# Kernel tuning notes

Hardware: AMD Instinct MI355X
Metric: run time of the kernel (lower is better)

Reference implementation:

```python
import jax, jax.numpy as jnp
import numpy as np

N_VARS = 28
HID = 64
BATCH = 32768
BN_EPS = 1e-5


def _lin_init(key, fan_in, shape):
    bound = 1.0 / np.sqrt(fan_in)
    return jax.random.uniform(key, shape, minval=-bound, maxval=bound, dtype=jnp.float32)


def setup_inputs() -> dict:
    key = jax.random.key(0)
    ks = jax.random.split(key, 8)
    n, h = N_VARS, HID
    X = jax.random.normal(ks[0], (BATCH, n), dtype=jnp.float32)
    W_logits = jax.random.uniform(ks[1], (n, n), minval=-0.01, maxval=0.01, dtype=jnp.float32)
    # per-mechanism (grouped) weights, stacked on leading mechanism axis n
    W1 = _lin_init(ks[2], n, (n, h, n)); b1 = _lin_init(ks[3], n, (n, h))
    W2 = _lin_init(ks[4], h, (n, h, h)); b2 = _lin_init(ks[5], h, (n, h))
    W3 = _lin_init(ks[6], h, (n, 1, h)); b3 = _lin_init(ks[7], h, (n, 1))
    gamma1 = jnp.ones((n, h)); beta1 = jnp.zeros((n, h))
    gamma2 = jnp.ones((n, h)); beta2 = jnp.zeros((n, h))
    return {"X": X, "W_logits": W_logits,
            "W1": W1, "b1": b1, "gamma1": gamma1, "beta1": beta1,
            "W2": W2, "b2": b2, "gamma2": gamma2, "beta2": beta2,
            "W3": W3, "b3": b3}


def _bn(x, gamma, beta):
    # x: [n, B, h]; batch stats over B (training-mode BatchNorm1d, biased var)
    m = x.mean(axis=1, keepdims=True)
    v = ((x - m) ** 2).mean(axis=1, keepdims=True)
    return gamma[:, None, :] * (x - m) * jax.lax.rsqrt(v + BN_EPS) + beta[:, None, :]


def reference(X, W_logits, W1, b1, gamma1, beta1, W2, b2, gamma2, beta2, W3, b3):
    n = W_logits.shape[0]
    # adjacency: sigmoid with zeroed diagonal
    W = jax.nn.sigmoid(W_logits) * (1.0 - jnp.eye(n, dtype=W_logits.dtype))
    # fuse the parent mask into the first layer's weights: one grouped GEMM
    # instead of n_vars separate masked matmuls
    W1_eff = W1 * W[:, None, :]                               # [n, h, n]
    h1 = jnp.einsum('bd,nhd->nbh', X, W1_eff) + b1[:, None, :]  # [n, B, h]
    a1 = jax.nn.gelu(_bn(h1, gamma1, beta1), approximate=False)
    h2 = jnp.einsum('nbh,ngh->nbg', a1, W2) + b2[:, None, :]
    a2 = jax.nn.gelu(_bn(h2, gamma2, beta2), approximate=False)
    out = jnp.einsum('nbh,noh->nbo', a2, W3) + b3[:, None, :]   # [n, B, 1]
    X_hat = out[:, :, 0].T                                     # [B, n]
    return (X_hat, W)
```

## Files before the change

### kernel.cpp

```cpp
#include <hip/hip_runtime.h>
#include <hip/hip_bf16.h>
#include <math.h>

typedef float  f4 __attribute__((ext_vector_type(4)));
typedef short  s8 __attribute__((ext_vector_type(8)));
typedef short  s4 __attribute__((ext_vector_type(4)));
typedef int    i2 __attribute__((ext_vector_type(2)));

#define NV 28
#define NB 32768
#define BN_EPS 1e-5f
#define NSLOT 434

#define SUM2_OFF   0
#define SSQ2_OFF   1792
#define BIAS1_OFF  3584
#define PART_OFF   9472
#define BF_BASE_F  120640
#define W2B_OFF_S  57344
#define XBF_OFF_S  172032
#define H2_BYTE_OFF 2924544ull
#define H2_BYTES    117440512ull

__device__ __forceinline__ float gelu_f(float x) {
    float x2 = x * x;
    float z  = x * __builtin_fmaf(x2, -0.10294324f, -2.3022082f);
    float t  = __builtin_amdgcn_exp2f(z);
    return x * __builtin_amdgcn_rcpf(1.0f + t);
}
__device__ __forceinline__ unsigned short f2bf(float x) {
    unsigned u = __builtin_bit_cast(unsigned, x);
    return (unsigned short)((u + 0x7fffu + ((u >> 16) & 1u)) >> 16);
}
__device__ __forceinline__ float bf2f(short s) {
    return __builtin_bit_cast(float, ((int)(unsigned short)s) << 16);
}
__device__ __forceinline__ int bfpack(float a, float b) {
    unsigned ua = __builtin_bit_cast(unsigned, a) + 0x8000u;
    unsigned ub = __builtin_bit_cast(unsigned, b) + 0x8000u;
    return __builtin_amdgcn_perm(ub, ua, 0x07060302);
}
__device__ __forceinline__ float row16_sum(float v) {
    int x;
    x = __builtin_amdgcn_update_dpp(0, __builtin_bit_cast(int, v), 0xB1, 0xF, 0xF, true);
    v += __builtin_bit_cast(float, x);
    x = __builtin_amdgcn_update_dpp(0, __builtin_bit_cast(int, v), 0x4E, 0xF, 0xF, true);
    v += __builtin_bit_cast(float, x);
    x = __builtin_amdgcn_update_dpp(0, __builtin_bit_cast(int, v), 0x124, 0xF, 0xF, true);
    v += __builtin_bit_cast(float, x);
    x = __builtin_amdgcn_update_dpp(0, __builtin_bit_cast(int, v), 0x128, 0xF, 0xF, true);
    v += __builtin_bit_cast(float, x);
    return v;
}
__device__ __forceinline__ float quad4_sum(float v) {
    int x;
    x = __builtin_amdgcn_update_dpp(0, __builtin_bit_cast(int, v), 0xB1, 0xF, 0xF, true);
    v += __builtin_bit_cast(float, x);
    x = __builtin_amdgcn_update_dpp(0, __builtin_bit_cast(int, v), 0x4E, 0xF, 0xF, true);
    v += __builtin_bit_cast(float, x);
    return v;
}

__global__ __launch_bounds__(256) void k_xstats(const float* __restrict__ X,
                                                float* __restrict__ ws) {
    __shared__ float sx[128 * 28];
    const int tid = threadIdx.x;
    const int rowbase = blockIdx.x * 128;
    {
        const f4* src = (const f4*)(X + (size_t)rowbase * 28);
        f4* dst = (f4*)sx;
        for (int i = tid; i < 128 * 28 / 4; i += 256) dst[i] = src[i];
    }
    __syncthreads();
    int* xb = (int*)((short*)(ws + BF_BASE_F) + XBF_OFF_S);
    for (int j = tid; j < 128 * 16; j += 256) {
        int row = j >> 4, cc = j & 15;
        float lo = (2 * cc     < 28) ? sx[row * 28 + 2 * cc]     : 0.0f;
        float hi = (2 * cc + 1 < 28) ? sx[row * 28 + 2 * cc + 1] : 0.0f;
        xb[(size_t)(rowbase + row) * 16 + cc] = (int)f2bf(lo) | ((int)f2bf(hi) << 16);
    }
    for (int s = tid; s < NSLOT; s += 256) {
        float a = 0.0f;
        if (s < 28) {
            for (int r = 0; r < 128; ++r) a += sx[r * 28 + s];
        } else {
            int p = s - 28, d = 0, rem = 28;
            while (p >= rem) { p -= rem; ++d; --rem; }
            int e = d + p;
            for (int r = 0; r < 128; ++r)
                a = __builtin_fmaf(sx[r * 28 + d], sx[r * 28 + e], a);
        }
        ws[PART_OFF + blockIdx.x * NSLOT + s] = a;
    }
}

__global__ __launch_bounds__(256) void k_fold1(const float* __restrict__ Wlog,
                                               const float* __restrict__ W1,
                                               const float* __restrict__ g1,
                                               const float* __restrict__ be1,
                                               const float* __restrict__ W2,
                                               float* __restrict__ ws,
                                               float* __restrict__ out_w) {
    __shared__ float sstat[NSLOT];
    __shared__ float mu[28], wrow[28];
    __shared__ float C[784];
    __shared__ float w1e_s[64 * 28];
    const int n = blockIdx.x, t = threadIdx.x;

    for (int s = t; s < NSLOT; s += 256) {
        float a = 0.0f;
#pragma unroll 16
        for (int p = 0; p < 256; ++p) a += ws[PART_OFF + p * NSLOT + s];
        sstat[s] = a;
    }
    if (t < 64) {
        ws[SUM2_OFF + n * 64 + t] = 0.0f;
        ws[SSQ2_OFF + n * 64 + t] = 0.0f;
    }
    __syncthreads();

    if (t < 28) {
        mu[t] = sstat[t] * (1.0f / 32768.0f);
        float w = 1.0f / (1.0f + expf(-Wlog[n * 28 + t]));
        if (t == n) w = 0.0f;
        wrow[t] = w;
        out_w[n * 28 + t] = w;
    }
    __syncthreads();
    for (int i = t; i < 784; i += 256) {
        int d = i / 28, e = i % 28;
        int lo = d < e ? d : e, hi = d < e ? e : d;
        int idx = 28 + lo * 28 - (lo * (lo - 1)) / 2 + (hi - lo);
        C[i] = sstat[idx] * (1.0f / 32768.0f) - mu[d] * mu[e];
    }
    for (int i = t; i < 1792; i += 256)
        w1e_s[i] = W1[(size_t)n * 1792 + i] * wrow[i % 28];
    __syncthreads();

    const int h = t >> 2, j = t & 3;
    const float* we = &w1e_s[h * 28];
    float var_p = 0.0f, dot_p = 0.0f;
#pragma unroll
    for (int k = 0; k < 7; ++k) {
        int d = 7 * j + k;
        float inner = 0.0f;
#pragma unroll
        for (int e = 0; e < 28; ++e) inner = __builtin_fmaf(C[d * 28 + e], we[e], inner);
        float wd = we[d];
        var_p = __builtin_fmaf(inner, wd, var_p);
        dot_p = __builtin_fmaf(wd, mu[d], dot_p);
    }
    float var  = quad4_sum(var_p);
    float dotm = quad4_sum(dot_p);
    float scale = g1[n * 64 + h] * rsqrtf(fmaxf(var, 0.0f) + BN_EPS);
    if (j == 0)
        ws[BIAS1_OFF + n * 64 + h] = be1[n * 64 + h] - dotm * scale;

    short* bfbase = (short*)(ws + BF_BASE_F);
    {
        short* w1f = bfbase + (size_t)(n * 64 + h) * 32;
        s8 pk;
#pragma unroll
        for (int k = 0; k < 8; ++k) {
            int d = 8 * j + k;
            pk[k] = (short)f2bf(d < 28 ? we[d] * scale : 0.0f);
        }
        *(s8*)&w1f[8 * j] = pk;
    }
    {
        const float* w2src = W2 + (size_t)n * 4096 + t * 16;
        short* w2d = bfbase + W2B_OFF_S + (size_t)n * 4096 + t * 16;
        s8 a, b;
#pragma unroll
        for (int k = 0; k < 8; ++k) a[k] = (short)f2bf(w2src[k]);
#pragma unroll
        for (int k = 0; k < 8; ++k) b[k] = (short)f2bf(w2src[8 + k]);
        *(s8*)&w2d[0] = a;
        *(s8*)&w2d[8] = b;
    }
}

template <bool STORE>
__global__ __launch_bounds__(256, 4) void k_pass1(float* __restrict__ ws,
                                                  short* __restrict__ h2buf) {
    __shared__ __align__(16) short sW1[64 * 40];
    __shared__ __align__(16) short sW2[64 * 72];
    __shared__ __align__(16) short sA1[8 * 16 * 72];
    __shared__ float sP1[4][64], sP2[4][64];

    const int n = blockIdx.x >> 7;
    const int blk = blockIdx.x & 127;
    const int tid = threadIdx.x;
    const int wave = tid >> 6;
    const int lane = tid & 63;
    const int m = lane & 15;
    const int q = lane >> 4;

    const short* bfbase = (const short*)(ws + BF_BASE_F);
    const short* w1g = bfbase + (size_t)n * 64 * 32;
    const short* w2g = bfbase + W2B_OFF_S + (size_t)n * 64 * 64;
    const short* xbf = bfbase + XBF_OFF_S;
    {
        int r = tid >> 2, c = tid & 3;
        *(s8*)&sW1[r * 40 + c * 8] = *(const s8*)&w1g[r * 32 + c * 8];
#pragma unroll
        for (int k = 0; k < 2; ++k) {
            int i2x = tid + k * 256;
            int r2 = i2x >> 3, c2 = i2x & 7;
            *(s8*)&sW2[r2 * 72 + c2 * 8] = *(const s8*)&w2g[r2 * 64 + c2 * 8];
        }
    }
    __syncthreads();

    const float* bias1 = ws + BIAS1_OFF + n * 64;
    f4 biasv[4];
#pragma unroll
    for (int t = 0; t < 4; ++t) biasv[t] = *(const f4*)&bias1[16 * t + 4 * q];

    short* myA1a = &sA1[(wave * 2 + 0) * 16 * 72];
    short* myA1b = &sA1[(wave * 2 + 1) * 16 * 72];
    float s1[16], s2v[16];
#pragma unroll
    for (int i = 0; i < 16; ++i) { s1[i] = 0.0f; s2v[i] = 0.0f; }

#pragma unroll
    for (int it = 0; it < 2; ++it) {
        const int row0 = blk * 256 + it * 128 + wave * 32;
        s8 xfa = *(const s8*)&xbf[(size_t)(row0 + m) * 32 + 8 * q];
        s8 xfb = *(const s8*)&xbf[(size_t)(row0 + 16 + m) * 32 + 8 * q];

        f4 acc1a[4], acc1b[4];
#pragma unroll
        for (int t = 0; t < 4; ++t) {
            s8 wf = *(const s8*)&sW1[(16 * t + m) * 40 + q * 8];
            acc1a[t] = __builtin_amdgcn_mfma_f32_16x16x32_bf16(wf, xfa, (f4){0.f, 0.f, 0.f, 0.f}, 0, 0, 0);
            acc1b[t] = __builtin_amdgcn_mfma_f32_16x16x32_bf16(wf, xfb, (f4){0.f, 0.f, 0.f, 0.f}, 0, 0, 0);
        }
#pragma unroll
        for (int t = 0; t < 4; ++t) {
            float ga0 = gelu_f(acc1a[t][0] + biasv[t][0]);
            float ga1 = gelu_f(acc1a[t][1] + biasv[t][1]);
            float ga2 = gelu_f(acc1a[t][2] + biasv[t][2]);
            float ga3 = gelu_f(acc1a[t][3] + biasv[t][3]);
            float gb0 = gelu_f(acc1b[t][0] + biasv[t][0]);
            float gb1 = gelu_f(acc1b[t][1] + biasv[t][1]);
            float gb2 = gelu_f(acc1b[t][2] + biasv[t][2]);
            float gb3 = gelu_f(acc1b[t][3] + biasv[t][3]);
            i2 pa = (i2){bfpack(ga0, ga1), bfpack(ga2, ga3)};
            i2 pb = (i2){bfpack(gb0, gb1), bfpack(gb2, gb3)};
            *(i2*)&myA1a[m * 72 + 16 * t + 4 * q] = pa;
            *(i2*)&myA1b[m * 72 + 16 * t + 4 * q] = pb;
        }
        s8 af0a = *(const s8*)&myA1a[m * 72 + 8 * q];
        s8 af1a = *(const s8*)&myA1a[m * 72 + 32 + 8 * q];
        s8 af0b = *(const s8*)&myA1b[m * 72 + 8 * q];
        s8 af1b = *(const s8*)&myA1b[m * 72 + 32 + 8 * q];
        short* hpA = STORE ? (h2buf + ((size_t)n * NB + row0 + m) * 64) : nullptr;
        short* hpB = STORE ? (h2buf + ((size_t)n * NB + row0 + 16 + m) * 64) : nullptr;
#pragma unroll
        for (int u = 0; u < 4; ++u) {
            s8 w0 = *(const s8*)&sW2[(16 * u + m) * 72 + 8 * q];
            s8 w1 = *(const s8*)&sW2[(16 * u + m) * 72 + 32 + 8 * q];
            f4 aa = (f4){0.f, 0.f, 0.f, 0.f};
            f4 ab = (f4){0.f, 0.f, 0.f, 0.f};
            aa = __builtin_amdgcn_mfma_f32_16x16x32_bf16(w0, af0a, aa, 0, 0, 0);
            ab = __builtin_amdgcn_mfma_f32_16x16x32_bf16(w0, af0b, ab, 0, 0, 0);
            aa = __builtin_amdgcn_mfma_f32_16x16x32_bf16(w1, af1a, aa, 0, 0, 0);
            ab = __builtin_amdgcn_mfma_f32_16x16x32_bf16(w1, af1b, ab, 0, 0, 0);
            if (STORE) {
                i2 ha = (i2){bfpack(aa[0], aa[1]), bfpack(aa[2], aa[3])};
                i2 hb = (i2){bfpack(ab[0], ab[1]), bfpack(ab[2], ab[3])};
                *(i2*)&hpA[16 * u + 4 * q] = ha;
                *(i2*)&hpB[16 * u + 4 * q] = hb;
            }
#pragma unroll
            for (int r = 0; r < 4; ++r) {
                s1[u * 4 + r]  += aa[r] + ab[r];
                s2v[u * 4 + r] = __builtin_fmaf(aa[r], aa[r], s2v[u * 4 + r]);
                s2v[u * 4 + r] = __builtin_fmaf(ab[r], ab[r], s2v[u * 4 + r]);
            }
        }
    }
#pragma unroll
    for (int u = 0; u < 4; ++u) {
#pragma unroll
        for (int r = 0; r < 4; ++r) {
            float t1 = row16_sum(s1[u * 4 + r]);
            float t2 = row16_sum(s2v[u * 4 + r]);
            if (m == 0) {
                sP1[wave][16 * u + 4 * q + r] = t1;
                sP2[wave][16 * u + 4 * q + r] = t2;
            }
        }
    }
    __syncthreads();
    if (tid < 64) {
        float a = sP1[0][tid] + sP1[1][tid] + sP1[2][tid] + sP1[3][tid];
        float b = sP2[0][tid] + sP2[1][tid] + sP2[2][tid] + sP2[3][tid];
        atomicAdd(&ws[SUM2_OFF + n * 64 + tid], a);
        atomicAdd(&ws[SSQ2_OFF + n * 64 + tid], b);
    }
}

__global__ __launch_bounds__(256) void k_pass2c(const float* __restrict__ g2,
                                                const float* __restrict__ be2,
                                                const float* __restrict__ W3,
                                                const float* __restrict__ b3,
                                                const float* __restrict__ ws,
                                                const short* __restrict__ h2buf,
                                                float* __restrict__ out) {
    __shared__ float sSc[64], sSh[64], sW3v[64];
    const int n = blockIdx.x >> 8;
    const int rbase = (blockIdx.x & 255) * 128;
    const int tid = threadIdx.x;
    if (tid < 64) {
        float mean = ws[SUM2_OFF + n * 64 + tid] * (1.0f / 32768.0f);
        float var  = ws[SSQ2_OFF + n * 64 + tid] * (1.0f / 32768.0f) - mean * mean;
        float sc = g2[n * 64 + tid] * rsqrtf(fmaxf(var, 0.0f) + BN_EPS);
        sSc[tid]  = sc;
        sSh[tid]  = be2[n * 64 + tid] - mean * sc;
        sW3v[tid] = W3[n * 64 + tid];
    }
    __syncthreads();
    const int wave = tid >> 6;
    const int lane = tid & 63;
    const int rr = lane >> 3;
    const int cc = lane & 7;
    f4 scA = *(const f4*)&sSc[cc * 8],     scB = *(const f4*)&sSc[cc * 8 + 4];
    f4 shA = *(const f4*)&sSh[cc * 8],     shB = *(const f4*)&sSh[cc * 8 + 4];
    f4 w3A = *(const f4*)&sW3v[cc * 8],    w3B = *(const f4*)&sW3v[cc * 8 + 4];
    const float b3n = b3[n];
#pragma unroll
    for (int it = 0; it < 4; ++it) {
        const int row = rbase + wave * 32 + it * 8 + rr;
        s8 hv = *(const s8*)(h2buf + ((size_t)n * NB + row) * 64 + cc * 8);
        float p = 0.0f;
#pragma unroll
        for (int j = 0; j < 4; ++j) {
            float v = __builtin_fmaf(bf2f(hv[j]), scA[j], shA[j]);
            p = __builtin_fmaf(gelu_f(v), w3A[j], p);
        }
#pragma unroll
        for (int j = 0; j < 4; ++j) {
            float v = __builtin_fmaf(bf2f(hv[4 + j]), scB[j], shB[j]);
            p = __builtin_fmaf(gelu_f(v), w3B[j], p);
        }
        p += __shfl_xor(p, 1);
        p += __shfl_xor(p, 2);
        p += __shfl_xor(p, 4);
        if (cc == 0) out[(size_t)row * 28 + n] = p + b3n;
    }
}

__global__ __launch_bounds__(256, 4) void k_pass2r(const float* __restrict__ g2,
                                                   const float* __restrict__ be2,
                                                   const float* __restrict__ W3,
                                                   const float* __restrict__ b3,
                                                   float* __restrict__ ws,
                                                   float* __restrict__ out) {
    __shared__ __align__(16) short sW1[64 * 40];
    __shared__ __align__(16) short sW2[64 * 72];
    __shared__ __align__(16) short sA1[8 * 16 * 72];
    __shared__ float sSc[64], sSh[64], sW3v[64];

    const int n = blockIdx.x >> 7;
    const int blk = blockIdx.x & 127;
    const int tid = threadIdx.x;
    const int wave = tid >> 6;
    const int lane = tid & 63;
    const int m = lane & 15;
    const int q = lane >> 4;

    const short* bfbase = (const short*)(ws + BF_BASE_F);
    const short* w1g = bfbase + (size_t)n * 64 * 32;
    const short* w2g = bfbase + W2B_OFF_S + (size_t)n * 64 * 64;
    const short* xbf = bfbase + XBF_OFF_S;
    {
        int r = tid >> 2, c = tid & 3;
        *(s8*)&sW1[r * 40 + c * 8] = *(const s8*)&w1g[r * 32 + c * 8];
#pragma unroll
        for (int k = 0; k < 2; ++k) {
            int i2x = tid + k * 256;
            int r2 = i2x >> 3, c2 = i2x & 7;
            *(s8*)&sW2[r2 * 72 + c2 * 8] = *(const s8*)&w2g[r2 * 64 + c2 * 8];
        }
        if (tid < 64) {
            float mean = ws[SUM2_OFF + n * 64 + tid] * (1.0f / 32768.0f);
            float var  = ws[SSQ2_OFF + n * 64 + tid] * (1.0f / 32768.0f) - mean * mean;
            float sc = g2[n * 64 + tid] * rsqrtf(fmaxf(var, 0.0f) + BN_EPS);
            sSc[tid]  = sc;
            sSh[tid]  = be2[n * 64 + tid] - mean * sc;
            sW3v[tid] = W3[n * 64 + tid];
        }
    }
    __syncthreads();

    const float* bias1 = ws + BIAS1_OFF + n * 64;
    const float b3n = b3[n];
    short* myA1a = &sA1[(wave * 2 + 0) * 16 * 72];
    short* myA1b = &sA1[(wave * 2 + 1) * 16 * 72];

#pragma unroll
    for (int it = 0; it < 2; ++it) {
        const int row0 = blk * 256 + it * 128 + wave * 32;
        s8 xfa = *(const s8*)&xbf[(size_t)(row0 + m) * 32 + 8 * q];
        s8 xfb = *(const s8*)&xbf[(size_t)(row0 + 16 + m) * 32 + 8 * q];

        f4 acc1a[4], acc1b[4];
#pragma unroll
        for (int t = 0; t < 4; ++t) {
            s8 wf = *(const s8*)&sW1[(16 * t + m) * 40 + q * 8];
            acc1a[t] = __builtin_amdgcn_mfma_f32_16x16x32_bf16(wf, xfa, (f4){0.f, 0.f, 0.f, 0.f}, 0, 0, 0);
            acc1b[t] = __builtin_amdgcn_mfma_f32_16x16x32_bf16(wf, xfb, (f4){0.f, 0.f, 0.f, 0.f}, 0, 0, 0);
        }
#pragma unroll
        for (int t = 0; t < 4; ++t) {
            f4 bv = *(const f4*)&bias1[16 * t + 4 * q];
            s4 pa, pb;
#pragma unroll
            for (int r = 0; r < 4; ++r) {
                pa[r] = (short)f2bf(gelu_f(acc1a[t][r] + bv[r]));
                pb[r] = (short)f2bf(gelu_f(acc1b[t][r] + bv[r]));
            }
            *(s4*)&myA1a[m * 72 + 16 * t + 4 * q] = pa;
            *(s4*)&myA1b[m * 72 + 16 * t + 4 * q] = pb;
        }
        s8 af0a = *(const s8*)&myA1a[m * 72 + 8 * q];
        s8 af1a = *(const s8*)&myA1a[m * 72 + 32 + 8 * q];
        s8 af0b = *(const s8*)&myA1b[m * 72 + 8 * q];
        s8 af1b = *(const s8*)&myA1b[m * 72 + 32 + 8 * q];
        float pa = 0.0f, pb = 0.0f;
#pragma unroll
        for (int u = 0; u < 4; ++u) {
            s8 w0 = *(const s8*)&sW2[(16 * u + m) * 72 + 8 * q];
            s8 w1 = *(const s8*)&sW2[(16 * u + m) * 72 + 32 + 8 * q];
            f4 aa = (f4){0.f, 0.f, 0.f, 0.f};
            f4 ab = (f4){0.f, 0.f, 0.f, 0.f};
            aa = __builtin_amdgcn_mfma_f32_16x16x32_bf16(w0, af0a, aa, 0, 0, 0);
            ab = __builtin_amdgcn_mfma_f32_16x16x32_bf16(w0, af0b, ab, 0, 0, 0);
            aa = __builtin_amdgcn_mfma_f32_16x16x32_bf16(w1, af1a, aa, 0, 0, 0);
            ab = __builtin_amdgcn_mfma_f32_16x16x32_bf16(w1, af1b, ab, 0, 0, 0);
            f4 scv = *(const f4*)&sSc[16 * u + 4 * q];
            f4 shv = *(const f4*)&sSh[16 * u + 4 * q];
            f4 w3v = *(const f4*)&sW3v[16 * u + 4 * q];
#pragma unroll
            for (int r = 0; r < 4; ++r) {
                float va = __builtin_fmaf(aa[r], scv[r], shv[r]);
                float vb = __builtin_fmaf(ab[r], scv[r], shv[r]);
                pa = __builtin_fmaf(gelu_f(va), w3v[r], pa);
                pb = __builtin_fmaf(gelu_f(vb), w3v[r], pb);
            }
        }
        pa += __shfl_xor(pa, 16);  pa += __shfl_xor(pa, 32);
        pb += __shfl_xor(pb, 16);  pb += __shfl_xor(pb, 32);
        if (q == 0) {
            out[(size_t)(row0 + m) * 28 + n]      = pa + b3n;
            out[(size_t)(row0 + 16 + m) * 28 + n] = pb + b3n;
        }
    }
}

extern "C" void kernel_launch(void* const* d_in, const int* in_sizes, int n_in,
                              void* d_out, int out_size, void* d_ws, size_t ws_size,
                              hipStream_t stream) {
    const float* X   = (const float*)d_in[0];
    const float* Wl  = (const float*)d_in[1];
    const float* W1  = (const float*)d_in[2];
    const float* g1  = (const float*)d_in[4];
    const float* be1 = (const float*)d_in[5];
    const float* W2  = (const float*)d_in[6];
    const float* g2  = (const float*)d_in[8];
    const float* be2 = (const float*)d_in[9];
    const float* W3  = (const float*)d_in[10];
    const float* b3  = (const float*)d_in[11];
    float* out = (float*)d_out;
    float* ws  = (float*)d_ws;
    short* h2buf = (short*)((char*)d_ws + H2_BYTE_OFF);
    const bool store_h2 = ws_size >= H2_BYTE_OFF + H2_BYTES;

    k_xstats<<<dim3(256), dim3(256), 0, stream>>>(X, ws);
    k_fold1<<<dim3(28), dim3(256), 0, stream>>>(Wl, W1, g1, be1, W2, ws, out + 917504);
    if (store_h2) {
        k_pass1<true><<<dim3(28 * 128), dim3(256), 0, stream>>>(ws, h2buf);
        k_pass2c<<<dim3(28 * 256), dim3(256), 0, stream>>>(g2, be2, W3, b3, ws, h2buf, out);
    } else {
        k_pass1<false><<<dim3(28 * 128), dim3(256), 0, stream>>>(ws, nullptr);
        k_pass2r<<<dim3(28 * 128), dim3(256), 0, stream>>>(g2, be2, W3, b3, ws, out);
    }
}
```

Before: 175.0 us.

## Derive layer-2 BN stats from a1 Gram matrix instead of materializing h2

Replaces the pass that computed h2 (and optionally stored it as bf16) to collect BatchNorm statistics with a kernel that accumulates the 64x64 Gram matrix and column sums of the GELU activations a1 via MFMA. A small fold kernel then computes the mean and variance of h2 = W2·a1 analytically as W2·mean and W2·Cov·W2ᵀ. The 117MB h2 buffer write/read and the layer-2 GEMM in the stats pass go away, and the recompute-based pass2r is always used for the output. The trade-off is extra Gram MFMA work, a partial-sum reduction, and a second recompute of layer 1 and layer 2 in pass2r, plus possible precision differences from the covariance formulation.

```diff
diff --git a/kernel.cpp b/kernel.cpp
--- a/kernel.cpp
+++ b/kernel.cpp
@@ -19,8 +19,7 @@
 #define BF_BASE_F  120640
 #define W2B_OFF_S  57344
 #define XBF_OFF_S  172032
-#define H2_BYTE_OFF 2924544ull
-#define H2_BYTES    117440512ull
+#define GRAMP_OFF  731136
 
 __device__ __forceinline__ float gelu_f(float x) {
     float x2 = x * x;
@@ -113,10 +112,6 @@
         for (int p = 0; p < 256; ++p) a += ws[PART_OFF + p * NSLOT + s];
         sstat[s] = a;
     }
-    if (t < 64) {
-        ws[SUM2_OFF + n * 64 + t] = 0.0f;
-        ws[SSQ2_OFF + n * 64 + t] = 0.0f;
-    }
     __syncthreads();
 
     if (t < 28) {
@@ -180,16 +175,10 @@
     }
 }
 
-template <bool STORE>
-__global__ __launch_bounds__(256, 4) void k_pass1(float* __restrict__ ws,
-                                                  short* __restrict__ h2buf) {
-    __shared__ __align__(16) short sW1[64 * 40];
-    __shared__ __align__(16) short sW2[64 * 72];
-    __shared__ __align__(16) short sA1[8 * 16 * 72];
-    __shared__ float sP1[4][64], sP2[4][64];
-
-    const int n = blockIdx.x >> 7;
-    const int blk = blockIdx.x & 127;
+__global__ __launch_bounds__(256, 3) void k_agram(float* __restrict__ ws) {
+    __shared__ __align__(16) char smem[21504];
+    const int n = blockIdx.x >> 5;
+    const int blk = blockIdx.x & 31;
     const int tid = threadIdx.x;
     const int wave = tid >> 6;
     const int lane = tid & 63;
@@ -198,157 +187,149 @@
 
     const short* bfbase = (const short*)(ws + BF_BASE_F);
     const short* w1g = bfbase + (size_t)n * 64 * 32;
-    const short* w2g = bfbase + W2B_OFF_S + (size_t)n * 64 * 64;
     const short* xbf = bfbase + XBF_OFF_S;
-    {
-        int r = tid >> 2, c = tid & 3;
-        *(s8*)&sW1[r * 40 + c * 8] = *(const s8*)&w1g[r * 32 + c * 8];
-#pragma unroll
-        for (int k = 0; k < 2; ++k) {
-            int i2x = tid + k * 256;
-            int r2 = i2x >> 3, c2 = i2x & 7;
-            *(s8*)&sW2[r2 * 72 + c2 * 8] = *(const s8*)&w2g[r2 * 64 + c2 * 8];
-        }
-    }
-    __syncthreads();
-
     const float* bias1 = ws + BIAS1_OFF + n * 64;
-    f4 biasv[4];
-#pragma unroll
-    for (int t = 0; t < 4; ++t) biasv[t] = *(const f4*)&bias1[16 * t + 4 * q];
-
-    short* myA1a = &sA1[(wave * 2 + 0) * 16 * 72];
-    short* myA1b = &sA1[(wave * 2 + 1) * 16 * 72];
-    float s1[16], s2v[16];
-#pragma unroll
-    for (int i = 0; i < 16; ++i) { s1[i] = 0.0f; s2v[i] = 0.0f; }
-
-#pragma unroll
-    for (int it = 0; it < 2; ++it) {
-        const int row0 = blk * 256 + it * 128 + wave * 32;
+
+    s8 wgf[4];
+    float bv[4];
+#pragma unroll
+    for (int u = 0; u < 4; ++u) {
+        wgf[u] = *(const s8*)&w1g[(16 * u + m) * 32 + 8 * q];
+        bv[u]  = bias1[16 * u + m];
+    }
+
+    short* T = (short*)(smem + wave * 5120);
+    f4 gram[10];
+#pragma unroll
+    for (int p = 0; p < 10; ++p) gram[p] = (f4){0.f, 0.f, 0.f, 0.f};
+    float csum[4] = {0.f, 0.f, 0.f, 0.f};
+
+#pragma unroll 1
+    for (int c = 0; c < 8; ++c) {
+        const int row0 = blk * 1024 + wave * 256 + c * 32;
         s8 xfa = *(const s8*)&xbf[(size_t)(row0 + m) * 32 + 8 * q];
         s8 xfb = *(const s8*)&xbf[(size_t)(row0 + 16 + m) * 32 + 8 * q];
-
-        f4 acc1a[4], acc1b[4];
-#pragma unroll
-        for (int t = 0; t < 4; ++t) {
-            s8 wf = *(const s8*)&sW1[(16 * t + m) * 40 + q * 8];
-            acc1a[t] = __builtin_amdgcn_mfma_f32_16x16x32_bf16(wf, xfa, (f4){0.f, 0.f, 0.f, 0.f}, 0, 0, 0);
-            acc1b[t] = __builtin_amdgcn_mfma_f32_16x16x32_bf16(wf, xfb, (f4){0.f, 0.f, 0.f, 0.f}, 0, 0, 0);
-        }
-#pragma unroll
-        for (int t = 0; t < 4; ++t) {
-            float ga0 = gelu_f(acc1a[t][0] + biasv[t][0]);
-            float ga1 = gelu_f(acc1a[t][1] + biasv[t][1]);
-            float ga2 = gelu_f(acc1a[t][2] + biasv[t][2]);
-            float ga3 = gelu_f(acc1a[t][3] + biasv[t][3]);
-            float gb0 = gelu_f(acc1b[t][0] + biasv[t][0]);
-            float gb1 = gelu_f(acc1b[t][1] + biasv[t][1]);
-            float gb2 = gelu_f(acc1b[t][2] + biasv[t][2]);
-            float gb3 = gelu_f(acc1b[t][3] + biasv[t][3]);
-            i2 pa = (i2){bfpack(ga0, ga1), bfpack(ga2, ga3)};
-            i2 pb = (i2){bfpack(gb0, gb1), bfpack(gb2, gb3)};
-            *(i2*)&myA1a[m * 72 + 16 * t + 4 * q] = pa;
-            *(i2*)&myA1b[m * 72 + 16 * t + 4 * q] = pb;
-        }
-        s8 af0a = *(const s8*)&myA1a[m * 72 + 8 * q];
-        s8 af1a = *(const s8*)&myA1a[m * 72 + 32 + 8 * q];
-        s8 af0b = *(const s8*)&myA1b[m * 72 + 8 * q];
-        s8 af1b = *(const s8*)&myA1b[m * 72 + 32 + 8 * q];
-        short* hpA = STORE ? (h2buf + ((size_t)n * NB + row0 + m) * 64) : nullptr;
-        short* hpB = STORE ? (h2buf + ((size_t)n * NB + row0 + 16 + m) * 64) : nullptr;
 #pragma unroll
         for (int u = 0; u < 4; ++u) {
-            s8 w0 = *(const s8*)&sW2[(16 * u + m) * 72 + 8 * q];
-            s8 w1 = *(const s8*)&sW2[(16 * u + m) * 72 + 32 + 8 * q];
-            f4 aa = (f4){0.f, 0.f, 0.f, 0.f};
-            f4 ab = (f4){0.f, 0.f, 0.f, 0.f};
-            aa = __builtin_amdgcn_mfma_f32_16x16x32_bf16(w0, af0a, aa, 0, 0, 0);
-            ab = __builtin_amdgcn_mfma_f32_16x16x32_bf16(w0, af0b, ab, 0, 0, 0);
-            aa = __builtin_amdgcn_mfma_f32_16x16x32_bf16(w1, af1a, aa, 0, 0, 0);
-            ab = __builtin_amdgcn_mfma_f32_16x16x32_bf16(w1, af1b, ab, 0, 0, 0);
-            if (STORE) {
-                i2 ha = (i2){bfpack(aa[0], aa[1]), bfpack(aa[2], aa[3])};
-                i2 hb = (i2){bfpack(ab[0], ab[1]), bfpack(ab[2], ab[3])};
-                *(i2*)&hpA[16 * u + 4 * q] = ha;
-                *(i2*)&hpB[16 * u + 4 * q] = hb;
-            }
-#pragma unroll
-            for (int r = 0; r < 4; ++r) {
-                s1[u * 4 + r]  += aa[r] + ab[r];
-                s2v[u * 4 + r] = __builtin_fmaf(aa[r], aa[r], s2v[u * 4 + r]);
-                s2v[u * 4 + r] = __builtin_fmaf(ab[r], ab[r], s2v[u * 4 + r]);
-            }
-        }
-    }
+            f4 ha = __builtin_amdgcn_mfma_f32_16x16x32_bf16(xfa, wgf[u], (f4){0.f,0.f,0.f,0.f}, 0, 0, 0);
+            f4 hb = __builtin_amdgcn_mfma_f32_16x16x32_bf16(xfb, wgf[u], (f4){0.f,0.f,0.f,0.f}, 0, 0, 0);
+            float g0 = gelu_f(ha[0] + bv[u]), g1 = gelu_f(ha[1] + bv[u]);
+            float g2 = gelu_f(ha[2] + bv[u]), g3 = gelu_f(ha[3] + bv[u]);
+            float e0 = gelu_f(hb[0] + bv[u]), e1 = gelu_f(hb[1] + bv[u]);
+            float e2 = gelu_f(hb[2] + bv[u]), e3 = gelu_f(hb[3] + bv[u]);
+            csum[u] += (g0 + g1 + g2 + g3) + (e0 + e1 + e2 + e3);
+            i2 pa = (i2){bfpack(g0, g1), bfpack(g2, g3)};
+            i2 pb = (i2){bfpack(e0, e1), bfpack(e2, e3)};
+            *(i2*)&T[(16 * u + m) * 40 + 4 * q]      = pa;
+            *(i2*)&T[(16 * u + m) * 40 + 16 + 4 * q] = pb;
+        }
+        s8 fr0 = *(const s8*)&T[(m)*40      + 8 * q];
+        s8 fr1 = *(const s8*)&T[(16 + m)*40 + 8 * q];
+        s8 fr2 = *(const s8*)&T[(32 + m)*40 + 8 * q];
+        s8 fr3 = *(const s8*)&T[(48 + m)*40 + 8 * q];
+        gram[0] = __builtin_amdgcn_mfma_f32_16x16x32_bf16(fr0, fr0, gram[0], 0, 0, 0);
+        gram[1] = __builtin_amdgcn_mfma_f32_16x16x32_bf16(fr0, fr1, gram[1], 0, 0, 0);
+        gram[2] = __builtin_amdgcn_mfma_f32_16x16x32_bf16(fr0, fr2, gram[2], 0, 0, 0);
+        gram[3] = __builtin_amdgcn_mfma_f32_16x16x32_bf16(fr0, fr3, gram[3], 0, 0, 0);
+        gram[4] = __builtin_amdgcn_mfma_f32_16x16x32_bf16(fr1, fr1, gram[4], 0, 0, 0);
+        gram[5] = __builtin_amdgcn_mfma_f32_16x16x32_bf16(fr1, fr2, gram[5], 0, 0, 0);
+        gram[6] = __builtin_amdgcn_mfma_f32_16x16x32_bf16(fr1, fr3, gram[6], 0, 0, 0);
+        gram[7] = __builtin_amdgcn_mfma_f32_16x16x32_bf16(fr2, fr2, gram[7], 0, 0, 0);
+        gram[8] = __builtin_amdgcn_mfma_f32_16x16x32_bf16(fr2, fr3, gram[8], 0, 0, 0);
+        gram[9] = __builtin_amdgcn_mfma_f32_16x16x32_bf16(fr3, fr3, gram[9], 0, 0, 0);
+    }
+
+    float* colbuf = (float*)(smem + 20480);
 #pragma unroll
     for (int u = 0; u < 4; ++u) {
-#pragma unroll
-        for (int r = 0; r < 4; ++r) {
-            float t1 = row16_sum(s1[u * 4 + r]);
-            float t2 = row16_sum(s2v[u * 4 + r]);
-            if (m == 0) {
-                sP1[wave][16 * u + 4 * q + r] = t1;
-                sP2[wave][16 * u + 4 * q + r] = t2;
-            }
-        }
-    }
-    __syncthreads();
-    if (tid < 64) {
-        float a = sP1[0][tid] + sP1[1][tid] + sP1[2][tid] + sP1[3][tid];
-        float b = sP2[0][tid] + sP2[1][tid] + sP2[2][tid] + sP2[3][tid];
-        atomicAdd(&ws[SUM2_OFF + n * 64 + tid], a);
-        atomicAdd(&ws[SSQ2_OFF + n * 64 + tid], b);
-    }
-}
-
-__global__ __launch_bounds__(256) void k_pass2c(const float* __restrict__ g2,
-                                                const float* __restrict__ be2,
-                                                const float* __restrict__ W3,
-                                                const float* __restrict__ b3,
-                                                const float* __restrict__ ws,
-                                                const short* __restrict__ h2buf,
-                                                float* __restrict__ out) {
-    __shared__ float sSc[64], sSh[64], sW3v[64];
-    const int n = blockIdx.x >> 8;
-    const int rbase = (blockIdx.x & 255) * 128;
-    const int tid = threadIdx.x;
-    if (tid < 64) {
-        float mean = ws[SUM2_OFF + n * 64 + tid] * (1.0f / 32768.0f);
-        float var  = ws[SSQ2_OFF + n * 64 + tid] * (1.0f / 32768.0f) - mean * mean;
-        float sc = g2[n * 64 + tid] * rsqrtf(fmaxf(var, 0.0f) + BN_EPS);
-        sSc[tid]  = sc;
-        sSh[tid]  = be2[n * 64 + tid] - mean * sc;
-        sW3v[tid] = W3[n * 64 + tid];
-    }
-    __syncthreads();
-    const int wave = tid >> 6;
-    const int lane = tid & 63;
-    const int rr = lane >> 3;
-    const int cc = lane & 7;
-    f4 scA = *(const f4*)&sSc[cc * 8],     scB = *(const f4*)&sSc[cc * 8 + 4];
-    f4 shA = *(const f4*)&sSh[cc * 8],     shB = *(const f4*)&sSh[cc * 8 + 4];
-    f4 w3A = *(const f4*)&sW3v[cc * 8],    w3B = *(const f4*)&sW3v[cc * 8 + 4];
-    const float b3n = b3[n];
-#pragma unroll
-    for (int it = 0; it < 4; ++it) {
-        const int row = rbase + wave * 32 + it * 8 + rr;
-        s8 hv = *(const s8*)(h2buf + ((size_t)n * NB + row) * 64 + cc * 8);
-        float p = 0.0f;
-#pragma unroll
-        for (int j = 0; j < 4; ++j) {
-            float v = __builtin_fmaf(bf2f(hv[j]), scA[j], shA[j]);
-            p = __builtin_fmaf(gelu_f(v), w3A[j], p);
-        }
-#pragma unroll
-        for (int j = 0; j < 4; ++j) {
-            float v = __builtin_fmaf(bf2f(hv[4 + j]), scB[j], shB[j]);
-            p = __builtin_fmaf(gelu_f(v), w3B[j], p);
-        }
-        p += __shfl_xor(p, 1);
-        p += __shfl_xor(p, 2);
-        p += __shfl_xor(p, 4);
-        if (cc == 0) out[(size_t)row * 28 + n] = p + b3n;
+        float s = csum[u];
+        s += __shfl_xor(s, 16);
+        s += __shfl_xor(s, 32);
+        if (q == 0) colbuf[wave * 64 + u * 16 + m] = s;
+    }
+    __syncthreads();
+    float* gb = (float*)smem + (wave & 1) * 2560;
+    if (wave < 2) {
+#pragma unroll
+        for (int p = 0; p < 10; ++p)
+#pragma unroll
+            for (int r = 0; r < 4; ++r)
+                gb[p * 256 + (4 * q + r) * 16 + m] = gram[p][r];
+    }
+    __syncthreads();
+    if (wave >= 2) {
+#pragma unroll
+        for (int p = 0; p < 10; ++p)
+#pragma unroll
+            for (int r = 0; r < 4; ++r)
+                gb[p * 256 + (4 * q + r) * 16 + m] += gram[p][r];
+    }
+    __syncthreads();
+    const float* g0b = (const float*)smem;
+    const float* g1b = (const float*)smem + 2560;
+    float* gp = ws + GRAMP_OFF + (size_t)(n * 32 + blk) * 2624;
+    for (int i = tid; i < 2560; i += 256) gp[i] = g0b[i] + g1b[i];
+    if (tid < 64)
+        gp[2560 + tid] = colbuf[tid] + colbuf[64 + tid] + colbuf[128 + tid] + colbuf[192 + tid];
+}
+
+__global__ __launch_bounds__(256) void k_fold2(const float* __restrict__ W2,
+                                               float* __restrict__ ws) {
+    __shared__ float gsum[2624];
+    __shared__ float Ca[4096];
+    __shared__ float sW2f[4096];
+    __shared__ float ma[64];
+    const int n = blockIdx.x, t = threadIdx.x;
+
+    for (int s = t; s < 2624; s += 256) {
+        float a = 0.0f;
+        const float* gp = ws + GRAMP_OFF + (size_t)n * 32 * 2624 + s;
+#pragma unroll 8
+        for (int b = 0; b < 32; ++b) a += gp[(size_t)b * 2624];
+        gsum[s] = a;
+    }
+    for (int i = t; i < 4096; i += 256)
+        sW2f[i] = bf2f((short)f2bf(W2[(size_t)n * 4096 + i]));
+    __syncthreads();
+    if (t < 64) ma[t] = gsum[2560 + t] * (1.0f / 32768.0f);
+    __syncthreads();
+    for (int idx = t; idx < 4096; idx += 256) {
+        int i = idx >> 6, j = idx & 63;
+        int v = i >> 4, w = j >> 4, ii = i & 15, jj = j & 15;
+        float g = (v <= w)
+            ? gsum[(v * 4 - ((v * (v + 1)) >> 1) + w) * 256 + ii * 16 + jj]
+            : gsum[(w * 4 - ((w * (w + 1)) >> 1) + v) * 256 + jj * 16 + ii];
+        Ca[idx] = g * (1.0f / 32768.0f) - ma[i] * ma[j];
+    }
+    __syncthreads();
+
+    const int h = t >> 2, j4 = t & 3;
+    f4 wreg[16];
+#pragma unroll
+    for (int j = 0; j < 16; ++j) wreg[j] = *(const f4*)&sW2f[h * 64 + 4 * j];
+    float vp = 0.0f, mp = 0.0f;
+#pragma unroll
+    for (int k = 0; k < 16; ++k) {
+        const int i = 16 * j4 + k;
+        float inner = 0.0f;
+        const f4* cr = (const f4*)&Ca[i * 64];
+#pragma unroll
+        for (int j = 0; j < 16; ++j) {
+            f4 c = cr[j], w = wreg[j];
+            inner = __builtin_fmaf(c[0], w[0],
+                    __builtin_fmaf(c[1], w[1],
+                    __builtin_fmaf(c[2], w[2],
+                    __builtin_fmaf(c[3], w[3], inner))));
+        }
+        float wi = sW2f[h * 64 + i];
+        vp = __builtin_fmaf(inner, wi, vp);
+        mp = __builtin_fmaf(wi, ma[i], mp);
+    }
+    float var  = quad4_sum(vp);
+    float mean = quad4_sum(mp);
+    if (j4 == 0) {
+        ws[SUM2_OFF + n * 64 + h] = mean * 32768.0f;
+        ws[SSQ2_OFF + n * 64 + h] = (var + mean * mean) * 32768.0f;
     }
 }
 
@@ -475,16 +456,10 @@
     const float* b3  = (const float*)d_in[11];
     float* out = (float*)d_out;
     float* ws  = (float*)d_ws;
-    short* h2buf = (short*)((char*)d_ws + H2_BYTE_OFF);
-    const bool store_h2 = ws_size >= H2_BYTE_OFF + H2_BYTES;
 
     k_xstats<<<dim3(256), dim3(256), 0, stream>>>(X, ws);
     k_fold1<<<dim3(28), dim3(256), 0, stream>>>(Wl, W1, g1, be1, W2, ws, out + 917504);
-    if (store_h2) {
-        k_pass1<true><<<dim3(28 * 128), dim3(256), 0, stream>>>(ws, h2buf);
-        k_pass2c<<<dim3(28 * 256), dim3(256), 0, stream>>>(g2, be2, W3, b3, ws, h2buf, out);
-    } else {
-        k_pass1<false><<<dim3(28 * 128), dim3(256), 0, stream>>>(ws, nullptr);
-        k_pass2r<<<dim3(28 * 128), dim3(256), 0, stream>>>(g2, be2, W3, b3, ws, out);
-    }
-}
+    k_agram<<<dim3(28 * 32), dim3(256), 0, stream>>>(ws);
+    k_fold2<<<dim3(28), dim3(256), 0, stream>>>(W2, ws);
+    k_pass2r<<<dim3(28 * 128), dim3(256), 0, stream>>>(g2, be2, W3, b3, ws, out);
+}
```

Result: slower. 223.2 us (+27.5%).
